# Performance work log

Measured on AMD Instinct MI355X. Metric: run time of the kernel, lower is better.

Reference implementation:

```python
import jax, jax.numpy as jnp
import numpy as np

D_MODEL = 1024
N_HEADS = 16
D_HEAD = D_MODEL // N_HEADS
B, S = 2, 2048


def setup_inputs() -> dict:
    key = jax.random.key(0)
    ks = jax.random.split(key, 7)
    query = jax.random.normal(ks[0], (B, S, D_MODEL), dtype=jnp.float32)
    k_in = jax.random.normal(ks[1], (B, S, D_MODEL), dtype=jnp.float32)
    v_in = jax.random.normal(ks[2], (B, S, D_MODEL), dtype=jnp.float32)
    # causal mask: True = attend allowed (torch code keeps where mask != 0)
    mask = jnp.tril(jnp.ones((S, S), dtype=bool))
    scale = 1.0 / np.sqrt(D_MODEL)
    Wq = jax.random.normal(ks[3], (D_MODEL, D_MODEL), dtype=jnp.float32) * scale
    Wk = jax.random.normal(ks[4], (D_MODEL, D_MODEL), dtype=jnp.float32) * scale
    Wv = jax.random.normal(ks[5], (D_MODEL, D_MODEL), dtype=jnp.float32) * scale
    Wo = jax.random.normal(ks[6], (D_MODEL, D_MODEL), dtype=jnp.float32) * scale
    return {"query": query, "key": k_in, "value": v_in, "mask": mask,
            "Wq": Wq, "Wk": Wk, "Wv": Wv, "Wo": Wo}


def reference(query, key, value, mask, Wq, Wk, Wv, Wo):
    b, sq, d = query.shape
    # bias-free linear: x @ W.T (torch nn.Linear convention)
    q = (query @ Wq.T).reshape(b, sq, N_HEADS, D_HEAD).transpose(0, 2, 1, 3)  # b h s d
    k = (key @ Wk.T).reshape(b, -1, N_HEADS, D_HEAD).transpose(0, 2, 1, 3)
    v = (value @ Wv.T).reshape(b, -1, N_HEADS, D_HEAD).transpose(0, 2, 1, 3)
    scores = jnp.einsum('bhqd,bhkd->bhqk', q, k) / jnp.sqrt(jnp.float32(D_HEAD))
    scores = jnp.where(mask[None, None, :, :], scores, jnp.float32(-1e9))
    attn = jax.nn.softmax(scores, axis=-1)
    # dropout is identity in eval mode
    ctx = jnp.einsum('bhqk,bhkd->bhqd', attn, v)
    ctx = ctx.transpose(0, 2, 1, 3).reshape(b, sq, d)
    return ctx @ Wo.T
```

## Files before the change

### kernel.cpp

```cpp
#include <hip/hip_runtime.h>
#include <hip/hip_bf16.h>
#include <cstdint>


typedef unsigned short u16;
typedef u16 u16x4 __attribute__((ext_vector_type(4)));
typedef u16 u16x8 __attribute__((ext_vector_type(8)));
typedef unsigned u32x2 __attribute__((ext_vector_type(2)));
typedef unsigned u32x4 __attribute__((ext_vector_type(4)));
typedef __bf16 bf16x8 __attribute__((ext_vector_type(8)));
typedef float f32x4 __attribute__((ext_vector_type(4)));

#define S_LEN 2048
#define DM 1024
#define NH 16
#define DH 64
#define BATCH 2
#define MTOT (BATCH*S_LEN)

__device__ __forceinline__ u16 f2bf(float f) {
  union { float f; unsigned u; } v; v.f = f;
  unsigned r = v.u + 0x7FFFu + ((v.u >> 16) & 1u);
  return (u16)(r >> 16);
}

__device__ __forceinline__ f32x4 mfma16(u16x8 a, u16x8 b, f32x4 c) {
  return __builtin_amdgcn_mfma_f32_16x16x32_bf16(
      __builtin_bit_cast(bf16x8, a), __builtin_bit_cast(bf16x8, b), c, 0, 0, 0);
}
__device__ __forceinline__ unsigned cvtpk_bf16(float lo, float hi) {
  unsigned r;
  asm("v_cvt_pk_bf16_f32 %0, %1, %2" : "=v"(r) : "v"(lo), "v"(hi));
  return r;
}
__device__ __forceinline__ void gload16(const u16* g, u16* l) {
  __builtin_amdgcn_global_load_lds(
      (const __attribute__((address_space(1))) unsigned int*)g,
      (__attribute__((address_space(3))) unsigned int*)l, 16, 0, 0);
}

__global__ __launch_bounds__(256) void cvt_kernel(
    const float* __restrict__ s0, const float* __restrict__ s1,
    const float* __restrict__ s2, const float* __restrict__ s3,
    u16* __restrict__ d0, u16* __restrict__ d1,
    u16* __restrict__ d2, u16* __restrict__ d3) {
  const int y = blockIdx.y;
  const float* s = (y == 0) ? s0 : (y == 1) ? s1 : (y == 2) ? s2 : s3;
  u16* d       = (y == 0) ? d0 : (y == 1) ? d1 : (y == 2) ? d2 : d3;
  int i = (blockIdx.x * 256 + threadIdx.x) * 4;
  f32x4 v = *(const f32x4*)&s[i];
  u16x4 o;
  o[0] = f2bf(v[0]); o[1] = f2bf(v[1]); o[2] = f2bf(v[2]); o[3] = f2bf(v[3]);
  *(u16x4*)&d[i] = o;
}

#define BM 128
#define BN 128
#define BKK 32

template<int MODE, bool AF32>
__device__ __forceinline__ void gemm_core(const void* __restrict__ Av,
                                          const u16* __restrict__ Bw,
                                          void* __restrict__ Cv,
                                          int K, float scale,
                                          int bx, int by, u16* smem) {
  const int BUFSZ = AF32 ? 12288 : 8192;
  const int AOFF  = AF32 ? 8192  : 4096;
  const u16* A16 = (const u16*)Av;
  const float* A32 = (const float*)Av;
  const int tid  = threadIdx.x;
  const int lane = tid & 63, w = tid >> 6;
  const int g = lane >> 4, r16 = lane & 15;
  const int wm = w >> 1, wn = w & 1;
  const int rowBase = by * BM;
  const int colBase = bx * BN;
  f32x4 acc[4][4] = {};

  const int srowB = lane >> 2;
  const int swzB  = ((lane & 3) ^ ((lane >> 3) & 3)) * 8;
  const u16* gB[2]; int oB[2];
#pragma unroll
  for (int j = 0; j < 2; j++) {
    const int c = w * 2 + j;
    gB[j] = &Bw[(size_t)(colBase + c * 16 + srowB) * K + swzB];
    oB[j] = c * 512;
  }
  const u16* gA16[2]; int oA16[2];
  const float* gA32[4]; int oA32[4];
  if constexpr (AF32) {
    const int srow8 = lane >> 3;
    const int scF   = ((lane & 7) ^ srow8) * 4;
#pragma unroll
    for (int j = 0; j < 4; j++) {
      const int rb = w * 32 + j * 8;
      gA32[j] = &A32[(size_t)(rowBase + rb + srow8) * K + scF];
      oA32[j] = rb * 32;
    }
  } else {
#pragma unroll
    for (int j = 0; j < 2; j++) {
      const int c = w * 2 + j;
      gA16[j] = &A16[(size_t)(rowBase + c * 16 + srowB) * K + swzB];
      oA16[j] = c * 512;
    }
  }

  const int NT = K / BKK;
  {
    u16* base = smem;
    if constexpr (AF32) {
      float* a32 = (float*)base;
#pragma unroll
      for (int j = 0; j < 4; j++) gload16((const u16*)gA32[j], (u16*)(a32 + oA32[j]));
    } else {
#pragma unroll
      for (int j = 0; j < 2; j++) gload16(gA16[j], base + oA16[j]);
    }
#pragma unroll
    for (int j = 0; j < 2; j++) gload16(gB[j], base + AOFF + oB[j]);
  }
  const int rswz = (r16 >> 1) & 3;
  int cur = 0;
  for (int t = 0; t < NT; ++t) {
    __syncthreads();
    if (t + 1 < NT) {
      const int k0 = (t + 1) * BKK;
      u16* base = smem + (cur ^ 1) * BUFSZ;
      if constexpr (AF32) {
        float* a32 = (float*)base;
#pragma unroll
        for (int j = 0; j < 4; j++) gload16((const u16*)(gA32[j] + k0), (u16*)(a32 + oA32[j]));
      } else {
#pragma unroll
        for (int j = 0; j < 2; j++) gload16(gA16[j] + k0, base + oA16[j]);
      }
#pragma unroll
      for (int j = 0; j < 2; j++) gload16(gB[j] + k0, base + AOFF + oB[j]);
    }
    u16* As = smem + cur * BUFSZ;
    u16* Bs = As + AOFF;
    float* As32 = (float*)As;
    u16x8 af[4], bfv[4];
    if constexpr (AF32) {
      const int rx = r16 & 7;
#pragma unroll
      for (int i = 0; i < 4; i++) {
        const int base_ = (wm * 64 + i * 16 + r16) * 32;
        f32x4 a0 = *(const f32x4*)&As32[base_ + (((g * 2)     ^ rx) * 4)];
        f32x4 a1 = *(const f32x4*)&As32[base_ + (((g * 2 + 1) ^ rx) * 4)];
        u32x4 wv = {cvtpk_bf16(a0[0], a0[1]), cvtpk_bf16(a0[2], a0[3]),
                    cvtpk_bf16(a1[0], a1[1]), cvtpk_bf16(a1[2], a1[3])};
        af[i] = __builtin_bit_cast(u16x8, wv);
      }
    } else {
#pragma unroll
      for (int i = 0; i < 4; i++)
        af[i] = *(const u16x8*)&As[(wm*64 + i*16 + r16) * BKK + ((g ^ rswz) * 8)];
    }
#pragma unroll
    for (int j = 0; j < 4; j++)
      bfv[j] = *(const u16x8*)&Bs[(wn*64 + j*16 + r16) * BKK + ((g ^ rswz) * 8)];
    __builtin_amdgcn_s_setprio(1);
#pragma unroll
    for (int i = 0; i < 4; i++)
#pragma unroll
      for (int j = 0; j < 4; j++) acc[i][j] = mfma16(af[i], bfv[j], acc[i][j]);
    __builtin_amdgcn_s_setprio(0);
    cur ^= 1;
  }
#pragma unroll
  for (int i = 0; i < 4; i++) {
#pragma unroll
    for (int j = 0; j < 4; j++) {
      int row = rowBase + wm*64 + i*16 + 4*g;
      int col = colBase + wn*64 + j*16 + r16;
      if (MODE == 0) {
        u16* O = (u16*)Cv;
        int head = col >> 6, d = col & 63;
#pragma unroll
        for (int r = 0; r < 4; r++)
          O[((size_t)head * MTOT + row + r) * DH + d] = f2bf(acc[i][j][r] * scale);
      } else if (MODE == 1) {
        u16x4 o;
#pragma unroll
        for (int r = 0; r < 4; r++) o[r] = f2bf(acc[i][j][r]);
        *(u16x4*)&((u16*)Cv)[(size_t)col * MTOT + row] = o;
      } else {
#pragma unroll
        for (int r = 0; r < 4; r++)
          ((float*)Cv)[(size_t)(row + r) * DM + col] = acc[i][j][r];
      }
    }
  }
}

__device__ __forceinline__ void gemm_remap(int& bx, int& by) {
  const int flat = blockIdx.x + 8 * blockIdx.y;
  const int xcd = flat & 7, i = flat >> 3;
  bx = i & 7;
  by = xcd * 4 + (i >> 3);
}

__global__ __launch_bounds__(256) void qkv_proj_kernel(
    const float* __restrict__ Xq, const float* __restrict__ Xk, const float* __restrict__ Xv,
    const u16* __restrict__ Wq, const u16* __restrict__ Wk, const u16* __restrict__ Wv,
    u16* __restrict__ Qp, u16* __restrict__ Kp, u16* __restrict__ Vt) {
  __shared__ u16 smem[24576];
  int bx, by; gemm_remap(bx, by);
  const int z = blockIdx.z;
  if (z == 0)      gemm_core<0, true>(Xq, Wq, Qp, DM, 0.125f * 1.44269504f, bx, by, smem);
  else if (z == 1) gemm_core<0, true>(Xk, Wk, Kp, DM, 1.0f, bx, by, smem);
  else             gemm_core<1, true>(Xv, Wv, Vt, DM, 1.0f, bx, by, smem);
}

__global__ __launch_bounds__(256) void out_proj_kernel(
    const u16* __restrict__ Ctx, const u16* __restrict__ Wo, float* __restrict__ Out) {
  __shared__ u16 smem[16384];
  int bx, by; gemm_remap(bx, by);
  gemm_core<2, false>(Ctx, Wo, Out, DM, 1.0f, bx, by, smem);
}


#define STAGE(B, T)                                                            \
  {                                                                            \
    const int kv0_ = (T) * 64;                                                 \
    _Pragma("unroll")                                                          \
    for (int j = 0; j < 2; j++) {                                              \
      const int rb = wv * 16 + j * 8;                                          \
      gload16(&Kbase[(size_t)(kv0_ + rb + srow) * DH + sc16 * 8],              \
              &Kl[B][rb * 64]);                                                \
      gload16(&Vbase[(size_t)(rb + srow) * MTOT + kv0_ + sc16 * 8],            \
              &Vl[B][rb * 64]);                                                \
    }                                                                          \
  }

#define TILE_BODY(BUF, T)                                                      \
  {                                                                            \
    const int kv0 = (T) * 64;                                                  \
    const f32x4 minit = {-16.f, -16.f, -16.f, -16.f};                          \
    f32x4 s[4] = {minit, minit, minit, minit};         \
    __builtin_amdgcn_s_setprio(1);                                             \
    _Pragma("unroll")                                                          \
    for (int f = 0; f < 4; f++) {                                              \
      _Pragma("unroll")                                                        \
      for (int ds = 0; ds < 2; ds++) {                                         \
        u16x8 kf = *(const u16x8*)&Kl[BUF][(f * 16 + q16) * 64 +               \
                                           ((ds * 4 + g) ^ qx7) * 8];          \
        s[f] = mfma16(kf, qf[ds], s[f]);                                       \
      }                                                                        \
    }                                                                          \
    __builtin_amdgcn_s_setprio(0);                                             \
    if ((T) == ntb - 1) {             \
      const int qg = qb16 + q16;                                               \
      _Pragma("unroll")                                                        \
      for (int f = 0; f < 4; f++)                                              \
        _Pragma("unroll")                                                      \
        for (int r = 0; r < 4; r++)                                            \
          if (kv0 + f * 16 + 4 * g + r > qg) s[f][r] = -1e30f;                 \
    }                                                                          \
    _Pragma("unroll")                                                          \
    for (int f = 0; f < 4; f++)                                                \
      _Pragma("unroll")                                                        \
      for (int r = 0; r < 4; r++) s[f][r] = exp2f(s[f][r]);                    \
            \
    _Pragma("unroll")                                                          \
    for (int f = 0; f < 4; f++) {                                              \
      const int cidx = (((2 * f + (g >> 1)) ^ qx7) * 8) + 4 * (g & 1);         \
      u32x2 pw = {cvtpk_bf16(s[f][0], s[f][1]), cvtpk_bf16(s[f][2], s[f][3])}; \
      *(u32x2*)&P16[q16 * 64 + cidx] = pw;                                     \
    }                                                                          \
    asm volatile("s_waitcnt lgkmcnt(0)" ::: "memory");                         \
    __builtin_amdgcn_sched_barrier(0);                                         \
    u16x8 pa0 = *(const u16x8*)&P16[q16 * 64 + ((g)     ^ qx7) * 8];           \
    u16x8 pa1 = *(const u16x8*)&P16[q16 * 64 + ((4 + g) ^ qx7) * 8];           \
    __builtin_amdgcn_s_setprio(1);                                             \
    lsum = mfma16(pa0, onesv, lsum);               \
    lsum = mfma16(pa1, onesv, lsum);                                           \
    _Pragma("unroll")                                                          \
    for (int dt = 0; dt < 4; dt++) {                                           \
      u16x8 vf0 = *(const u16x8*)&Vl[BUF][(dt * 16 + q16) * 64 +               \
                                          ((g)     ^ qx7) * 8];                \
      u16x8 vf1 = *(const u16x8*)&Vl[BUF][(dt * 16 + q16) * 64 +               \
                                          ((4 + g) ^ qx7) * 8];                \
      ctx[dt] = mfma16(pa0, vf0, ctx[dt]);                                     \
      ctx[dt] = mfma16(pa1, vf1, ctx[dt]);                                     \
    }                                                                          \
    __builtin_amdgcn_s_setprio(0);                                             \
  }

__global__ __launch_bounds__(256, 4) void attn_kernel(const u16* __restrict__ Qp,
                                                      const u16* __restrict__ Kp,
                                                      const u16* __restrict__ Vt,
                                                      u16* __restrict__ Ctx) {
  __shared__ u16 Kl[2][64 * 64];
  __shared__ u16 Vl[2][64 * 64];
  __shared__ u16 Pl[4][16 * 64];
  const int tid = threadIdx.x;
  const int lane = tid & 63, wv = tid >> 6;
  const int q16 = lane & 15, g = lane >> 4;
  const int qx7 = q16 & 7;
  const int flat = blockIdx.x;
  const int xcd = flat & 7, idx = flat >> 3;
  const int bh = xcd * 4 + (idx & 3);
  const int qc = 31 - (idx >> 2);
  const int bb = bh >> 4, h = bh & 15;
  const int qb16 = qc * 64 + wv * 16;

  const u16* Qbase = Qp + (size_t)(h * MTOT + bb * S_LEN) * DH;
  const u16* Kbase = Kp + (size_t)(h * MTOT + bb * S_LEN) * DH;
  const u16* Vbase = Vt + (size_t)(h * DH) * MTOT + bb * S_LEN;
  u16* P16 = Pl[wv];

  u16x8 qf[2];
#pragma unroll
  for (int ds = 0; ds < 2; ds++)
    qf[ds] = *(const u16x8*)&Qbase[(size_t)(qb16 + q16) * DH + ds * 32 + g * 8];

  f32x4 ctx[4] = {};
  f32x4 lsum = {};
  const u16x8 onesv = {0x3F80, 0x3F80, 0x3F80, 0x3F80,
                       0x3F80, 0x3F80, 0x3F80, 0x3F80};
  const int ntb = qc + 1;

  const int srow = lane >> 3;
  const int sc16 = (lane & 7) ^ srow;

  STAGE(0, 0);
  int cur = 0;
  for (int t = 0; t < ntb; ++t) {
    __syncthreads();
    if (t + 1 < ntb) STAGE(cur ^ 1, t + 1);
    TILE_BODY(cur, t);
    cur ^= 1;
  }

  float inv[4];
#pragma unroll
  for (int r = 0; r < 4; r++) inv[r] = 1.f / lsum[r];
#pragma unroll
  for (int dt = 0; dt < 4; dt++)
#pragma unroll
    for (int r = 0; r < 4; r++) {
      size_t grow = (size_t)(bb * S_LEN + qb16 + 4 * g + r) * DM + h * DH;
      Ctx[grow + dt * 16 + q16] = f2bf(ctx[dt][r] * inv[r]);
    }
}

extern "C" void kernel_launch(void* const* d_in, const int* in_sizes, int n_in,
                              void* d_out, int out_size, void* d_ws, size_t ws_size,
                              hipStream_t stream) {
  const float* q_in = (const float*)d_in[0];
  const float* k_in = (const float*)d_in[1];
  const float* v_in = (const float*)d_in[2];
  const float* wq = (const float*)d_in[4];
  const float* wk = (const float*)d_in[5];
  const float* wv = (const float*)d_in[6];
  const float* wo = (const float*)d_in[7];

  char* ws = (char*)d_ws;
  const size_t MB = 1024ull * 1024ull;
  u16* Qp  = (u16*)(ws + 0  * MB);
  u16* Kp  = (u16*)(ws + 8  * MB);
  u16* Vt  = (u16*)(ws + 16 * MB);
  u16* Ctx = (u16*)(ws + 24 * MB);
  u16* Wqb = (u16*)(ws + 56 * MB);
  u16* Wkb = (u16*)(ws + 58 * MB);
  u16* Wvb = (u16*)(ws + 60 * MB);
  u16* Wob = (u16*)(ws + 62 * MB);

  cvt_kernel<<<dim3(DM * DM / 1024, 4), 256, 0, stream>>>(
      wq, wk, wv, wo, Wqb, Wkb, Wvb, Wob);
  qkv_proj_kernel<<<dim3(8, MTOT / BM, 3), 256, 0, stream>>>(
      q_in, k_in, v_in, Wqb, Wkb, Wvb, Qp, Kp, Vt);
  attn_kernel<<<dim3(1024), 256, 0, stream>>>(Qp, Kp, Vt, Ctx);
  out_proj_kernel<<<dim3(8, MTOT / BM), 256, 0, stream>>>(Ctx, Wob, (float*)d_out);
}
```

Baseline: 107.2 us.

## Triple-buffer GEMM tiles with explicit vmcnt waits and two-tile prefetch

```diff
diff --git a/kernel.cpp b/kernel.cpp
--- a/kernel.cpp
+++ b/kernel.cpp
@@ -105,37 +105,42 @@
     }
   }
 
+#define STAGE_TILE(BASE, K0)                                                   \
+  {                                                                            \
+    u16* base_ = (BASE);                                                       \
+    if constexpr (AF32) {                                                      \
+      float* a32_ = (float*)base_;                                             \
+      _Pragma("unroll")                                                        \
+      for (int j = 0; j < 4; j++)                                              \
+        gload16((const u16*)(gA32[j] + (K0)), (u16*)(a32_ + oA32[j]));         \
+    } else {                                                                   \
+      _Pragma("unroll")                                                        \
+      for (int j = 0; j < 2; j++)                                              \
+        gload16(gA16[j] + (K0), base_ + oA16[j]);                              \
+    }                                                                          \
+    _Pragma("unroll")                                                          \
+    for (int j = 0; j < 2; j++)                                                \
+      gload16(gB[j] + (K0), base_ + AOFF + oB[j]);                             \
+  }
+
   const int NT = K / BKK;
-  {
-    u16* base = smem;
-    if constexpr (AF32) {
-      float* a32 = (float*)base;
-#pragma unroll
-      for (int j = 0; j < 4; j++) gload16((const u16*)gA32[j], (u16*)(a32 + oA32[j]));
-    } else {
-#pragma unroll
-      for (int j = 0; j < 2; j++) gload16(gA16[j], base + oA16[j]);
-    }
-#pragma unroll
-    for (int j = 0; j < 2; j++) gload16(gB[j], base + AOFF + oB[j]);
-  }
+  STAGE_TILE(smem, 0);
+  STAGE_TILE(smem + BUFSZ, BKK);
+
   const int rswz = (r16 >> 1) & 3;
   int cur = 0;
   for (int t = 0; t < NT; ++t) {
-    __syncthreads();
     if (t + 1 < NT) {
-      const int k0 = (t + 1) * BKK;
-      u16* base = smem + (cur ^ 1) * BUFSZ;
-      if constexpr (AF32) {
-        float* a32 = (float*)base;
-#pragma unroll
-        for (int j = 0; j < 4; j++) gload16((const u16*)(gA32[j] + k0), (u16*)(a32 + oA32[j]));
-      } else {
-#pragma unroll
-        for (int j = 0; j < 2; j++) gload16(gA16[j] + k0, base + oA16[j]);
-      }
-#pragma unroll
-      for (int j = 0; j < 2; j++) gload16(gB[j] + k0, base + AOFF + oB[j]);
+      if constexpr (AF32) asm volatile("s_waitcnt vmcnt(6)" ::: "memory");
+      else                asm volatile("s_waitcnt vmcnt(4)" ::: "memory");
+    } else {
+      asm volatile("s_waitcnt vmcnt(0)" ::: "memory");
+    }
+    __builtin_amdgcn_s_barrier();
+    __builtin_amdgcn_sched_barrier(0);
+    if (t + 2 < NT) {
+      const int pfb = (cur + 2 >= 3) ? cur - 1 : cur + 2;
+      STAGE_TILE(smem + pfb * BUFSZ, (t + 2) * BKK);
     }
     u16* As = smem + cur * BUFSZ;
     u16* Bs = As + AOFF;
@@ -166,8 +171,9 @@
 #pragma unroll
       for (int j = 0; j < 4; j++) acc[i][j] = mfma16(af[i], bfv[j], acc[i][j]);
     __builtin_amdgcn_s_setprio(0);
-    cur ^= 1;
-  }
+    cur = (cur == 2) ? 0 : cur + 1;
+  }
+#undef STAGE_TILE
 #pragma unroll
   for (int i = 0; i < 4; i++) {
 #pragma unroll
@@ -205,7 +211,7 @@
     const float* __restrict__ Xq, const float* __restrict__ Xk, const float* __restrict__ Xv,
     const u16* __restrict__ Wq, const u16* __restrict__ Wk, const u16* __restrict__ Wv,
     u16* __restrict__ Qp, u16* __restrict__ Kp, u16* __restrict__ Vt) {
-  __shared__ u16 smem[24576];
+  __shared__ u16 smem[36864];
   int bx, by; gemm_remap(bx, by);
   const int z = blockIdx.z;
   if (z == 0)      gemm_core<0, true>(Xq, Wq, Qp, DM, 0.125f * 1.44269504f, bx, by, smem);
@@ -215,7 +221,7 @@
 
 __global__ __launch_bounds__(256) void out_proj_kernel(
     const u16* __restrict__ Ctx, const u16* __restrict__ Wo, float* __restrict__ Out) {
-  __shared__ u16 smem[16384];
+  __shared__ u16 smem[24576];
   int bx, by; gemm_remap(bx, by);
   gemm_core<2, false>(Ctx, Wo, Out, DM, 1.0f, bx, by, smem);
 }
```

Measured after the change: 109.6 us. +2.2%, slower.
